# Performance work log

Hardware: AMD Instinct MI355X
Metric: run time of the kernel (lower is better)

## Reference

```python
import jax, jax.numpy as jnp
import numpy as np

D_MODEL, D_HIDDEN, N_EXPERTS, TOP_K = 1024, 2048, 8, 2
B, T = 4, 2048


def setup_inputs() -> dict:
    key = jax.random.key(0)
    ks = jax.random.split(key, 9)
    s_d = 1.0 / np.sqrt(D_MODEL)
    s_h = 1.0 / np.sqrt(D_HIDDEN)
    return {
        "x": jax.random.normal(ks[0], (B, T, D_MODEL), jnp.float32),
        "gate_w": jax.random.normal(ks[1], (D_MODEL, N_EXPERTS), jnp.float32) * s_d,
        "gate_b": jnp.zeros((N_EXPERTS,), jnp.float32),
        "w1": jax.random.normal(ks[2], (N_EXPERTS, D_MODEL, D_HIDDEN), jnp.float32) * s_d,
        "b1": jnp.zeros((N_EXPERTS, D_HIDDEN), jnp.float32),
        "w2": jax.random.normal(ks[3], (N_EXPERTS, D_MODEL, D_HIDDEN), jnp.float32) * s_d,
        "b2": jnp.zeros((N_EXPERTS, D_HIDDEN), jnp.float32),
        "w3": jax.random.normal(ks[4], (N_EXPERTS, D_HIDDEN, D_MODEL), jnp.float32) * s_h,
        "b3": jnp.zeros((N_EXPERTS, D_MODEL), jnp.float32),
    }


def _moe_forward(x, gate_w, gate_b, w1, b1, w2, b2, w3, b3):
    # Router: [B, T, E]
    router_logits = x @ gate_w + gate_b
    top_k_logits, top_k_indices = jax.lax.top_k(router_logits, TOP_K)  # [B,T,K]
    top_k_probs = jax.nn.softmax(top_k_logits, axis=-1)

    # Dense all-expert SwiGLU (matches original, which runs every expert on full batch)
    h = jax.nn.silu(jnp.einsum('btd,edh->bteh', x, w1) + b1) * (
        jnp.einsum('btd,edh->bteh', x, w2) + b2)
    expert_out = jnp.einsum('bteh,ehd->bted', h, w3) + b3  # [B,T,E,D]

    # Combine: gather routed experts' outputs and weight by top-k probs
    gathered = jnp.take_along_axis(expert_out, top_k_indices[:, :, :, None], axis=2)  # [B,T,K,D]
    output = jnp.sum(top_k_probs[:, :, :, None] * gathered, axis=2)

    # Load-balance auxiliary loss
    gate_probs = jax.nn.softmax(router_logits, axis=-1).reshape(-1, N_EXPERTS)
    importance = gate_probs.mean(axis=0)
    idx_flat = top_k_indices.reshape(-1)
    load = jnp.bincount(idx_flat, length=N_EXPERTS).astype(jnp.float32) / idx_flat.size
    aux_loss = jnp.sum(importance * load) * N_EXPERTS
    return output, aux_loss


def reference(x, gate_w, gate_b, w1, b1, w2, b2, w3, b3):
    return _moe_forward(x, gate_w, gate_b, w1, b1, w2, b2, w3, b3)
```

## Files before the change

kernel.cpp:

```cpp
#include <hip/hip_runtime.h>
#include <stdint.h>


#define NTOK     8192
#define DM       1024
#define DH       2048
#define NEXP     8
#define NPAIR    16384
#define TILE_M   128
#define GRID_M   136
#define WC_ROWS  (GRID_M * TILE_M)

typedef _Float16 half8 __attribute__((ext_vector_type(8)));
typedef float    f32x4 __attribute__((ext_vector_type(4)));
typedef unsigned int u32;

__device__ __forceinline__ void gload16(const void* g, void* l) {
  __builtin_amdgcn_global_load_lds(
      (const __attribute__((address_space(1))) u32*)g,
      (__attribute__((address_space(3))) u32*)l, 16, 0, 0);
}

__global__ void init_kernel(float4* __restrict__ out4, int n4, float* __restrict__ aux,
                            int* __restrict__ rtok, float* __restrict__ rprob,
                            int* __restrict__ ctrl) {
  int gid = blockIdx.x * 256 + threadIdx.x;
  int stride = gridDim.x * 256;
  float4 z4 = {0.f, 0.f, 0.f, 0.f};
  for (int i = gid; i < n4; i += stride) out4[i] = z4;
  for (int i = gid; i < WC_ROWS; i += stride) { rtok[i] = -1; rprob[i] = 0.f; }
  if (gid < 64) ctrl[gid] = 0;
  if (gid == 0) *aux = 0.f;
}

template <bool SPLIT>
__global__ __launch_bounds__(256) void transpose_cvt_kernel(
    const float* __restrict__ w1, const float* __restrict__ w2, const float* __restrict__ w3,
    _Float16* __restrict__ w1h, _Float16* __restrict__ w1l,
    _Float16* __restrict__ w2h, _Float16* __restrict__ w2l,
    _Float16* __restrict__ w3h, _Float16* __restrict__ w3l) {
  int z = blockIdx.z;
  int R = (z == 2) ? DH : DM;
  int C = (z == 2) ? DM : DH;
  const float* in = (z == 0) ? w1 : (z == 1) ? w2 : w3;
  _Float16* outh  = (z == 0) ? w1h : (z == 1) ? w2h : w3h;
  _Float16* outl  = (z == 0) ? w1l : (z == 1) ? w2l : w3l;
  size_t ebase = (size_t)blockIdx.y * R * C;
  in += ebase;
  int tilesC = C >> 5;
  int tr = blockIdx.x / tilesC, tc = blockIdx.x % tilesC;
  int r0 = tr << 7, c0 = tc << 5;
  __shared__ float tsh[32][129];
  int tx = threadIdx.x, ty = threadIdx.y;
#pragma unroll
  for (int i = 0; i < 16; i++) {
    int r = ty + i * 8;
    tsh[tx][r] = in[(size_t)(r0 + r) * C + c0 + tx];
  }
  __syncthreads();
  int tid = ty * 32 + tx;
  int c = tid >> 3, g = tid & 7;
  const float* trow = &tsh[c][g * 16];
  _Float16 thi[16], tlo[16];
#pragma unroll
  for (int j = 0; j < 16; j++) {
    float v = trow[j];
    _Float16 hi = (_Float16)v;
    thi[j] = hi;
    if (SPLIT) tlo[j] = (_Float16)(v - (float)hi);
  }
  size_t dsto = ebase + (size_t)(c0 + c) * R + r0 + g * 16;
  half8* dh = (half8*)(outh + dsto);
  dh[0] = *(half8*)&thi[0];
  dh[1] = *(half8*)&thi[8];
  if (SPLIT) {
    half8* dl = (half8*)(outl + dsto);
    dl[0] = *(half8*)&tlo[0];
    dl[1] = *(half8*)&tlo[8];
  }
}

template <bool SPLIT>
__global__ __launch_bounds__(256) void router_kernel(
    const float* __restrict__ x, const float* __restrict__ gw, const float* __restrict__ gb,
    float* __restrict__ g_imp, int* __restrict__ g_cnt,
    int* __restrict__ tok_e, float* __restrict__ tok_p,
    _Float16* __restrict__ xhi, _Float16* __restrict__ xlo) {
  __shared__ float s_imp[8];
  __shared__ int   s_cnt[8];
  int t = threadIdx.x;
  if (t < 8) { s_imp[t] = 0.f; s_cnt[t] = 0; }
  __syncthreads();
  int wave = t >> 6, lane = t & 63;
  int tok = blockIdx.x * 4 + wave;
  const float4* xr = (const float4*)(x + (size_t)tok * DM);
  float acc[8] = {0.f,0.f,0.f,0.f,0.f,0.f,0.f,0.f};
  _Float16 hh[16], ll[16];
#pragma unroll
  for (int j = 0; j < 4; j++) {
    float4 v = xr[lane * 4 + j];
    const float* gw0 = gw + (size_t)(lane * 16 + j * 4) * 8;
#pragma unroll
    for (int e = 0; e < 8; e++)
      acc[e] += v.x * gw0[e] + v.y * gw0[8 + e] + v.z * gw0[16 + e] + v.w * gw0[24 + e];
    float vv[4] = {v.x, v.y, v.z, v.w};
#pragma unroll
    for (int q = 0; q < 4; q++) {
      _Float16 hi = (_Float16)vv[q];
      hh[j * 4 + q] = hi;
      if (SPLIT) ll[j * 4 + q] = (_Float16)(vv[q] - (float)hi);
    }
  }
  size_t xoff = (size_t)tok * DM + lane * 16;
  half8* xo = (half8*)(xhi + xoff);
  xo[0] = *(half8*)&hh[0];
  xo[1] = *(half8*)&hh[8];
  if (SPLIT) {
    half8* xl = (half8*)(xlo + xoff);
    xl[0] = *(half8*)&ll[0];
    xl[1] = *(half8*)&ll[8];
  }
#pragma unroll
  for (int off = 32; off > 0; off >>= 1) {
#pragma unroll
    for (int e = 0; e < 8; e++) acc[e] += __shfl_xor(acc[e], off, 64);
  }
  if (lane == 0) {
    float l[8];
#pragma unroll
    for (int e = 0; e < 8; e++) l[e] = acc[e] + gb[e];
    float v0 = l[0]; int i0 = 0;
#pragma unroll
    for (int e = 1; e < 8; e++) if (l[e] > v0) { v0 = l[e]; i0 = e; }
    float v1 = -3.4e38f; int i1 = -1;
#pragma unroll
    for (int e = 0; e < 8; e++) {
      if (e != i0 && l[e] > v1) { v1 = l[e]; i1 = e; }
    }
    float s = 0.f, p[8];
#pragma unroll
    for (int e = 0; e < 8; e++) { p[e] = expf(l[e] - v0); s += p[e]; }
    float inv = 1.f / s;
#pragma unroll
    for (int e = 0; e < 8; e++) atomicAdd(&s_imp[e], p[e] * inv);
    float e1 = expf(v1 - v0);
    float p0 = 1.f / (1.f + e1);
    tok_e[tok * 2] = i0;  tok_e[tok * 2 + 1] = i1;
    tok_p[tok * 2] = p0;  tok_p[tok * 2 + 1] = e1 * p0;
    atomicAdd(&s_cnt[i0], 1); atomicAdd(&s_cnt[i1], 1);
  }
  __syncthreads();
  if (t < 8) { atomicAdd(&g_imp[t], s_imp[t]); atomicAdd(&g_cnt[t], s_cnt[t]); }
}

__global__ void offsets_aux_kernel(const float* __restrict__ g_imp, const int* __restrict__ g_cnt,
                                   int* __restrict__ segoff, float* __restrict__ aux_out) {
  if (threadIdx.x == 0 && blockIdx.x == 0) {
    int off = 0;
    segoff[0] = 0;
    double aux = 0.0;
    for (int e = 0; e < 8; e++) {
      off += ((g_cnt[e] + TILE_M - 1) >> 7) << 7;
      segoff[e + 1] = off;
      aux += (double)g_imp[e] * (double)g_cnt[e];
    }
    aux_out[0] = (float)(aux * 8.0 / ((double)NTOK * (double)NPAIR));
  }
}

__global__ __launch_bounds__(256) void scatter_rows_kernel(
    const int* __restrict__ tok_e, const float* __restrict__ tok_p,
    const int* __restrict__ segoff, int* __restrict__ cursor,
    int* __restrict__ rtok, float* __restrict__ rprob, int* __restrict__ inv) {
  __shared__ int lcnt[8], lbase[8];
  int t = threadIdx.x;
  if (t < 8) lcnt[t] = 0;
  __syncthreads();
  int i = blockIdx.x * 256 + t;
  int e = tok_e[i];
  int lpos = atomicAdd(&lcnt[e], 1);
  __syncthreads();
  if (t < 8) lbase[t] = (lcnt[t] > 0) ? atomicAdd(&cursor[t], lcnt[t]) : 0;
  __syncthreads();
  int r = segoff[e] + lbase[e] + lpos;
  rtok[r]  = i >> 1;
  rprob[r] = tok_p[i];
  inv[i]   = r;
}

template <bool SPLIT>
__global__ __launch_bounds__(256) void gemm1_kernel(
    const _Float16* __restrict__ xhi, const _Float16* __restrict__ xlo,
    const _Float16* __restrict__ w1h, const _Float16* __restrict__ w1l,
    const _Float16* __restrict__ w2h, const _Float16* __restrict__ w2l,
    const float* __restrict__ b1, const float* __restrict__ b2,
    const int* __restrict__ rtok, const int* __restrict__ segoff,
    _Float16* __restrict__ hhi, _Float16* __restrict__ hlo) {
  int dflat = blockIdx.y * 136 + blockIdx.x;
  int xcd = dflat & 7, j = dflat >> 3;
  int wy = xcd * 2 + (j >= 136 ? 1 : 0);
  int wx = (j >= 136) ? j - 136 : j;
  int mbase = wx * TILE_M;
  if (mbase >= segoff[8]) return;
  int e = 0;
  while (mbase >= segoff[e + 1]) e++;
  int nbase = wy * 128;

  extern __shared__ char smem[];
  _Float16* Ah  = (_Float16*)smem;
  _Float16* B1h = Ah  + 4096;
  _Float16* B2h = B1h + 4096;
  _Float16* Al  = B2h + 4096;
  _Float16* B1l = Al  + 4096;
  _Float16* B2l = B1l + 4096;

  int t = threadIdx.x;
  int lane = t & 63, wave = t >> 6;
  int wr = wave >> 1, wc = wave & 1;

  int r0 = t >> 2, part = t & 3;
  int r1 = 64 + r0;
  int tokA0 = rtok[mbase + r0]; if (tokA0 < 0) tokA0 = 0;
  int tokA1 = rtok[mbase + r1]; if (tokA1 < 0) tokA1 = 0;
  size_t offA0 = (size_t)tokA0 * DM + part * 8;
  size_t offA1 = (size_t)tokA1 * DM + part * 8;
  size_t offB0 = ((size_t)e * DH + nbase + r0) * DM + part * 8;
  size_t offB1 = ((size_t)e * DH + nbase + r1) * DM + part * 8;
  int l0 = wave * 1024, l1 = 4096 + wave * 1024;

  f32x4 uacc[4][4], vacc[4][4];
#pragma unroll
  for (int a = 0; a < 4; a++)
#pragma unroll
    for (int b = 0; b < 4; b++) { uacc[a][b] = {0.f,0.f,0.f,0.f}; vacc[a][b] = {0.f,0.f,0.f,0.f}; }

  for (int kk = 0; kk < DM; kk += 32) {
    gload16(xhi + offA0 + kk, (char*)Ah  + l0);
    gload16(xhi + offA1 + kk, (char*)Ah  + l1);
    gload16(w1h + offB0 + kk, (char*)B1h + l0);
    gload16(w1h + offB1 + kk, (char*)B1h + l1);
    gload16(w2h + offB0 + kk, (char*)B2h + l0);
    gload16(w2h + offB1 + kk, (char*)B2h + l1);
    if (SPLIT) {
      gload16(xlo + offA0 + kk, (char*)Al  + l0);
      gload16(xlo + offA1 + kk, (char*)Al  + l1);
      gload16(w1l + offB0 + kk, (char*)B1l + l0);
      gload16(w1l + offB1 + kk, (char*)B1l + l1);
      gload16(w2l + offB0 + kk, (char*)B2l + l0);
      gload16(w2l + offB1 + kk, (char*)B2l + l1);
    }
    __syncthreads();
    int kpos = (lane >> 4) * 8;
    half8 ah[4], al[4];
#pragma unroll
    for (int i = 0; i < 4; i++) {
      int rowA = wr * 64 + i * 16 + (lane & 15);
      ah[i] = *(const half8*)&Ah[rowA * 32 + kpos];
      if (SPLIT) al[i] = *(const half8*)&Al[rowA * 32 + kpos];
    }
    {
      half8 bh[4], bl[4];
#pragma unroll
      for (int i = 0; i < 4; i++) {
        int rowB = wc * 64 + i * 16 + (lane & 15);
        bh[i] = *(const half8*)&B1h[rowB * 32 + kpos];
        if (SPLIT) bl[i] = *(const half8*)&B1l[rowB * 32 + kpos];
      }
#pragma unroll
      for (int mi = 0; mi < 4; mi++)
#pragma unroll
        for (int ni = 0; ni < 4; ni++) {
          uacc[mi][ni] = __builtin_amdgcn_mfma_f32_16x16x32_f16(ah[mi], bh[ni], uacc[mi][ni], 0, 0, 0);
          if (SPLIT) {
            uacc[mi][ni] = __builtin_amdgcn_mfma_f32_16x16x32_f16(ah[mi], bl[ni], uacc[mi][ni], 0, 0, 0);
            uacc[mi][ni] = __builtin_amdgcn_mfma_f32_16x16x32_f16(al[mi], bh[ni], uacc[mi][ni], 0, 0, 0);
          }
        }
    }
    {
      half8 bh[4], bl[4];
#pragma unroll
      for (int i = 0; i < 4; i++) {
        int rowB = wc * 64 + i * 16 + (lane & 15);
        bh[i] = *(const half8*)&B2h[rowB * 32 + kpos];
        if (SPLIT) bl[i] = *(const half8*)&B2l[rowB * 32 + kpos];
      }
#pragma unroll
      for (int mi = 0; mi < 4; mi++)
#pragma unroll
        for (int ni = 0; ni < 4; ni++) {
          vacc[mi][ni] = __builtin_amdgcn_mfma_f32_16x16x32_f16(ah[mi], bh[ni], vacc[mi][ni], 0, 0, 0);
          if (SPLIT) {
            vacc[mi][ni] = __builtin_amdgcn_mfma_f32_16x16x32_f16(ah[mi], bl[ni], vacc[mi][ni], 0, 0, 0);
            vacc[mi][ni] = __builtin_amdgcn_mfma_f32_16x16x32_f16(al[mi], bh[ni], vacc[mi][ni], 0, 0, 0);
          }
        }
    }
    __syncthreads();
  }

  const float* b1e = b1 + (size_t)e * DH;
  const float* b2e = b2 + (size_t)e * DH;
#pragma unroll
  for (int mi = 0; mi < 4; mi++)
#pragma unroll
    for (int ni = 0; ni < 4; ni++)
#pragma unroll
      for (int r = 0; r < 4; r++) {
        int row = mbase + wr * 64 + mi * 16 + (lane >> 4) * 4 + r;
        int col = nbase + wc * 64 + ni * 16 + (lane & 15);
        float u = uacc[mi][ni][r] + b1e[col];
        float v = vacc[mi][ni][r] + b2e[col];
        float hv = u / (1.f + expf(-u)) * v;
        _Float16 hi = (_Float16)hv;
        hhi[(size_t)row * DH + col] = hi;
        if (SPLIT) hlo[(size_t)row * DH + col] = (_Float16)(hv - (float)hi);
      }
}

template <bool SPLIT, bool WRITE_Y>
__global__ __launch_bounds__(256) void gemm2_kernel(
    const _Float16* __restrict__ hhi, const _Float16* __restrict__ hlo,
    const _Float16* __restrict__ w3h, const _Float16* __restrict__ w3l,
    const float* __restrict__ b3, const int* __restrict__ rtok,
    const float* __restrict__ rprob, const int* __restrict__ segoff,
    float* __restrict__ ybuf, float* __restrict__ out) {
  int dflat = blockIdx.y * 136 + blockIdx.x;
  int xcd = dflat & 7, j = dflat >> 3;
  int mbase = j * TILE_M;
  if (mbase >= segoff[8]) return;
  int e = 0;
  while (mbase >= segoff[e + 1]) e++;
  int nbase = xcd * 128;

  extern __shared__ char smem[];
  _Float16* Ah = (_Float16*)smem;
  _Float16* Bh = Ah + 4096;
  _Float16* Al = Bh + 4096;
  _Float16* Bl = Al + 4096;

  int t = threadIdx.x;
  int lane = t & 63, wave = t >> 6;
  int wr = wave >> 1, wc = wave & 1;

  int r0 = t >> 2, part = t & 3;
  int r1 = 64 + r0;
  size_t offA0 = (size_t)(mbase + r0) * DH + part * 8;
  size_t offA1 = (size_t)(mbase + r1) * DH + part * 8;
  size_t offB0 = ((size_t)e * DM + nbase + r0) * DH + part * 8;
  size_t offB1 = ((size_t)e * DM + nbase + r1) * DH + part * 8;
  int l0 = wave * 1024, l1 = 4096 + wave * 1024;

  f32x4 acc[4][4];
#pragma unroll
  for (int a = 0; a < 4; a++)
#pragma unroll
    for (int b = 0; b < 4; b++) acc[a][b] = {0.f,0.f,0.f,0.f};

  for (int kk = 0; kk < DH; kk += 32) {
    gload16(hhi + offA0 + kk, (char*)Ah + l0);
    gload16(hhi + offA1 + kk, (char*)Ah + l1);
    gload16(w3h + offB0 + kk, (char*)Bh + l0);
    gload16(w3h + offB1 + kk, (char*)Bh + l1);
    if (SPLIT) {
      gload16(hlo + offA0 + kk, (char*)Al + l0);
      gload16(hlo + offA1 + kk, (char*)Al + l1);
      gload16(w3l + offB0 + kk, (char*)Bl + l0);
      gload16(w3l + offB1 + kk, (char*)Bl + l1);
    }
    __syncthreads();
    int kpos = (lane >> 4) * 8;
    half8 ah[4], al[4], bh[4], bl[4];
#pragma unroll
    for (int i = 0; i < 4; i++) {
      int rowA = wr * 64 + i * 16 + (lane & 15);
      int rowB = wc * 64 + i * 16 + (lane & 15);
      ah[i] = *(const half8*)&Ah[rowA * 32 + kpos];
      bh[i] = *(const half8*)&Bh[rowB * 32 + kpos];
      if (SPLIT) {
        al[i] = *(const half8*)&Al[rowA * 32 + kpos];
        bl[i] = *(const half8*)&Bl[rowB * 32 + kpos];
      }
    }
#pragma unroll
    for (int mi = 0; mi < 4; mi++)
#pragma unroll
      for (int ni = 0; ni < 4; ni++) {
        acc[mi][ni] = __builtin_amdgcn_mfma_f32_16x16x32_f16(ah[mi], bh[ni], acc[mi][ni], 0, 0, 0);
        if (SPLIT) {
          acc[mi][ni] = __builtin_amdgcn_mfma_f32_16x16x32_f16(ah[mi], bl[ni], acc[mi][ni], 0, 0, 0);
          acc[mi][ni] = __builtin_amdgcn_mfma_f32_16x16x32_f16(al[mi], bh[ni], acc[mi][ni], 0, 0, 0);
        }
      }
    __syncthreads();
  }

  const float* b3e = b3 + (size_t)e * DM;
#pragma unroll
  for (int mi = 0; mi < 4; mi++)
#pragma unroll
    for (int r = 0; r < 4; r++) {
      int row = mbase + wr * 64 + mi * 16 + (lane >> 4) * 4 + r;
      if (WRITE_Y) {
#pragma unroll
        for (int ni = 0; ni < 4; ni++) {
          int col = nbase + wc * 64 + ni * 16 + (lane & 15);
          ybuf[(size_t)row * DM + col] = acc[mi][ni][r] + b3e[col];
        }
      } else {
        int tok = rtok[row];
        if (tok < 0) continue;
        float pr = rprob[row];
#pragma unroll
        for (int ni = 0; ni < 4; ni++) {
          int col = nbase + wc * 64 + ni * 16 + (lane & 15);
          float val = (acc[mi][ni][r] + b3e[col]) * pr;
          atomicAdd(&out[(size_t)tok * DM + col], val);
        }
      }
    }
}

__global__ __launch_bounds__(256) void combine_kernel(
    const float4* __restrict__ ybuf, const int* __restrict__ inv,
    const float* __restrict__ tok_p, float4* __restrict__ out) {
  int gid = blockIdx.x * 256 + threadIdx.x;
  int tok = gid >> 8;
  int c4  = gid & 255;
  int r0 = inv[tok * 2], r1 = inv[tok * 2 + 1];
  float p0 = tok_p[tok * 2], p1 = tok_p[tok * 2 + 1];
  float4 a = ybuf[(size_t)r0 * 256 + c4];
  float4 b = ybuf[(size_t)r1 * 256 + c4];
  float4 o;
  o.x = p0 * a.x + p1 * b.x;
  o.y = p0 * a.y + p1 * b.y;
  o.z = p0 * a.z + p1 * b.z;
  o.w = p0 * a.w + p1 * b.w;
  out[gid] = o;
}

extern "C" void kernel_launch(void* const* d_in, const int* in_sizes, int n_in,
                              void* d_out, int out_size, void* d_ws, size_t ws_size,
                              hipStream_t stream) {
  const float* x      = (const float*)d_in[0];
  const float* gate_w = (const float*)d_in[1];
  const float* gate_b = (const float*)d_in[2];
  const float* w1     = (const float*)d_in[3];
  const float* b1     = (const float*)d_in[4];
  const float* w2     = (const float*)d_in[5];
  const float* b2     = (const float*)d_in[6];
  const float* w3     = (const float*)d_in[7];
  const float* b3     = (const float*)d_in[8];
  float* out = (float*)d_out;

  const size_t SZ_XH = (size_t)NTOK * DM * 2;
  const size_t SZ_W  = (size_t)NEXP * DM * DH * 2;
  const size_t SZ_H  = (size_t)WC_ROWS * DH * 2;
  const size_t SZ_Y  = (size_t)WC_ROWS * DM * 4;
  const size_t SZ_RT = (size_t)WC_ROWS * 4;
  const size_t SZ_NP = (size_t)NPAIR * 4;

  char* ws = (char*)d_ws;
  float* g_imp  = (float*)(ws + 0);
  int*   g_cnt  = (int*)(ws + 32);
  int*   cursor = (int*)(ws + 64);
  int*   segoff = (int*)(ws + 96);

  size_t o = 256;
  _Float16 *A_xhi, *A_xlo, *A_w1h, *A_w1l, *A_w2h, *A_w2l, *A_w3h, *A_w3l, *A_hhi, *A_hlo;
  int *A_rtok, *A_toke, *A_inv; float *A_rprob, *A_tokp, *A_y;
  A_xhi = (_Float16*)(ws + o); o += SZ_XH;
  A_xlo = (_Float16*)(ws + o); o += SZ_XH;
  A_w1h = (_Float16*)(ws + o); o += SZ_W;
  A_w1l = (_Float16*)(ws + o); o += SZ_W;
  A_w2h = (_Float16*)(ws + o); o += SZ_W;
  A_w2l = (_Float16*)(ws + o); o += SZ_W;
  A_w3h = (_Float16*)(ws + o); o += SZ_W;
  A_w3l = (_Float16*)(ws + o); o += SZ_W;
  A_hhi = (_Float16*)(ws + o); o += SZ_H;
  A_hlo = (_Float16*)(ws + o); o += SZ_H;
  A_rtok = (int*)(ws + o);   o += SZ_RT;
  A_rprob= (float*)(ws + o); o += SZ_RT;
  A_toke = (int*)(ws + o);   o += SZ_NP;
  A_tokp = (float*)(ws + o); o += SZ_NP;
  A_inv  = (int*)(ws + o);   o += SZ_NP;
  A_y    = (float*)(ws + o); o += SZ_Y;
  size_t offA = o;

  o = 256;
  _Float16 *B_xh, *B_w1, *B_w2, *B_w3, *B_h;
  int *B_rtok, *B_toke, *B_inv; float *B_rprob, *B_tokp, *B_y;
  B_xh = (_Float16*)(ws + o); o += SZ_XH;
  B_w1 = (_Float16*)(ws + o); o += SZ_W;
  B_w2 = (_Float16*)(ws + o); o += SZ_W;
  B_w3 = (_Float16*)(ws + o); o += SZ_W;
  B_h  = (_Float16*)(ws + o); o += SZ_H;
  B_rtok = (int*)(ws + o);   o += SZ_RT;
  B_rprob= (float*)(ws + o); o += SZ_RT;
  B_toke = (int*)(ws + o);   o += SZ_NP;
  B_tokp = (float*)(ws + o); o += SZ_NP;
  B_inv  = (int*)(ws + o);   o += SZ_NP;
  size_t offC = o;
  B_y    = (float*)(ws + o); o += SZ_Y;
  size_t offB = o;

  int mode = (ws_size >= offA) ? 2 : (ws_size >= offB) ? 1 : 0;
  (void)offC;

  if (mode == 2) {
    init_kernel<<<2048, 256, 0, stream>>>((float4*)out, NTOK * DM / 4,
                                          out + (size_t)NTOK * DM, A_rtok, A_rprob, (int*)ws);
    transpose_cvt_kernel<true><<<dim3(512, 8, 3), dim3(32, 8), 0, stream>>>(
        w1, w2, w3, A_w1h, A_w1l, A_w2h, A_w2l, A_w3h, A_w3l);
    router_kernel<true><<<NTOK / 4, 256, 0, stream>>>(x, gate_w, gate_b, g_imp, g_cnt,
                                                      A_toke, A_tokp, A_xhi, A_xlo);
    offsets_aux_kernel<<<1, 64, 0, stream>>>(g_imp, g_cnt, segoff, out + (size_t)NTOK * DM);
    scatter_rows_kernel<<<NPAIR / 256, 256, 0, stream>>>(A_toke, A_tokp, segoff, cursor,
                                                         A_rtok, A_rprob, A_inv);
    gemm1_kernel<true><<<dim3(136, 16), 256, 49152, stream>>>(
        A_xhi, A_xlo, A_w1h, A_w1l, A_w2h, A_w2l, b1, b2, A_rtok, segoff, A_hhi, A_hlo);
    gemm2_kernel<true, true><<<dim3(136, 8), 256, 32768, stream>>>(
        A_hhi, A_hlo, A_w3h, A_w3l, b3, A_rtok, A_rprob, segoff, A_y, out);
    combine_kernel<<<NTOK * DM / 4 / 256, 256, 0, stream>>>((const float4*)A_y, A_inv,
                                                            A_tokp, (float4*)out);
  } else {
    init_kernel<<<2048, 256, 0, stream>>>((float4*)out, NTOK * DM / 4,
                                          out + (size_t)NTOK * DM, B_rtok, B_rprob, (int*)ws);
    transpose_cvt_kernel<false><<<dim3(512, 8, 3), dim3(32, 8), 0, stream>>>(
        w1, w2, w3, B_w1, nullptr, B_w2, nullptr, B_w3, nullptr);
    router_kernel<false><<<NTOK / 4, 256, 0, stream>>>(x, gate_w, gate_b, g_imp, g_cnt,
                                                       B_toke, B_tokp, B_xh, nullptr);
    offsets_aux_kernel<<<1, 64, 0, stream>>>(g_imp, g_cnt, segoff, out + (size_t)NTOK * DM);
    scatter_rows_kernel<<<NPAIR / 256, 256, 0, stream>>>(B_toke, B_tokp, segoff, cursor,
                                                         B_rtok, B_rprob, B_inv);
    gemm1_kernel<false><<<dim3(136, 16), 256, 24576, stream>>>(
        B_xh, nullptr, B_w1, nullptr, B_w2, nullptr, b1, b2, B_rtok, segoff, B_h, nullptr);
    if (mode == 1) {
      gemm2_kernel<false, true><<<dim3(136, 8), 256, 16384, stream>>>(
          B_h, nullptr, B_w3, nullptr, b3, B_rtok, B_rprob, segoff, B_y, out);
      combine_kernel<<<NTOK * DM / 4 / 256, 256, 0, stream>>>((const float4*)B_y, B_inv,
                                                              B_tokp, (float4*)out);
    } else {
      gemm2_kernel<false, false><<<dim3(136, 8), 256, 16384, stream>>>(
          B_h, nullptr, B_w3, nullptr, b3, B_rtok, B_rprob, segoff, B_y, out);
    }
  }
}
```

Baseline: 822.2 us.

## Drop split-fp16 compensation, double-buffer LDS with swizzle in both GEMMs

Removes the hi/lo fp16 split path, so the GEMMs run one MFMA per tile instead of three and move half the operand bytes. Both GEMMs gain double-buffered LDS staging with prefetch of the next K slice, an XOR swizzle on global-to-LDS placement against bank conflicts, and s_setprio around the MFMA blocks. SiLU now uses __expf. The trade is lower accuracy, since plain fp16 inputs replace the compensated product and may push results past the tolerance.

```diff
diff --git a/kernel.cpp b/kernel.cpp
--- a/kernel.cpp
+++ b/kernel.cpp
@@ -33,18 +33,14 @@
   if (gid == 0) *aux = 0.f;
 }
 
-template <bool SPLIT>
 __global__ __launch_bounds__(256) void transpose_cvt_kernel(
     const float* __restrict__ w1, const float* __restrict__ w2, const float* __restrict__ w3,
-    _Float16* __restrict__ w1h, _Float16* __restrict__ w1l,
-    _Float16* __restrict__ w2h, _Float16* __restrict__ w2l,
-    _Float16* __restrict__ w3h, _Float16* __restrict__ w3l) {
+    _Float16* __restrict__ w1t, _Float16* __restrict__ w2t, _Float16* __restrict__ w3t) {
   int z = blockIdx.z;
   int R = (z == 2) ? DH : DM;
   int C = (z == 2) ? DM : DH;
   const float* in = (z == 0) ? w1 : (z == 1) ? w2 : w3;
-  _Float16* outh  = (z == 0) ? w1h : (z == 1) ? w2h : w3h;
-  _Float16* outl  = (z == 0) ? w1l : (z == 1) ? w2l : w3l;
+  _Float16*   out = (z == 0) ? w1t : (z == 1) ? w2t : w3t;
   size_t ebase = (size_t)blockIdx.y * R * C;
   in += ebase;
   int tilesC = C >> 5;
@@ -61,31 +57,18 @@
   int tid = ty * 32 + tx;
   int c = tid >> 3, g = tid & 7;
   const float* trow = &tsh[c][g * 16];
-  _Float16 thi[16], tlo[16];
-#pragma unroll
-  for (int j = 0; j < 16; j++) {
-    float v = trow[j];
-    _Float16 hi = (_Float16)v;
-    thi[j] = hi;
-    if (SPLIT) tlo[j] = (_Float16)(v - (float)hi);
-  }
-  size_t dsto = ebase + (size_t)(c0 + c) * R + r0 + g * 16;
-  half8* dh = (half8*)(outh + dsto);
-  dh[0] = *(half8*)&thi[0];
-  dh[1] = *(half8*)&thi[8];
-  if (SPLIT) {
-    half8* dl = (half8*)(outl + dsto);
-    dl[0] = *(half8*)&tlo[0];
-    dl[1] = *(half8*)&tlo[8];
-  }
-}
-
-template <bool SPLIT>
+  _Float16 tmp[16];
+#pragma unroll
+  for (int j = 0; j < 16; j++) tmp[j] = (_Float16)trow[j];
+  half8* dst = (half8*)(out + ebase + (size_t)(c0 + c) * R + r0 + g * 16);
+  dst[0] = *(half8*)&tmp[0];
+  dst[1] = *(half8*)&tmp[8];
+}
+
 __global__ __launch_bounds__(256) void router_kernel(
     const float* __restrict__ x, const float* __restrict__ gw, const float* __restrict__ gb,
     float* __restrict__ g_imp, int* __restrict__ g_cnt,
-    int* __restrict__ tok_e, float* __restrict__ tok_p,
-    _Float16* __restrict__ xhi, _Float16* __restrict__ xlo) {
+    int* __restrict__ tok_e, float* __restrict__ tok_p, _Float16* __restrict__ xh) {
   __shared__ float s_imp[8];
   __shared__ int   s_cnt[8];
   int t = threadIdx.x;
@@ -95,7 +78,7 @@
   int tok = blockIdx.x * 4 + wave;
   const float4* xr = (const float4*)(x + (size_t)tok * DM);
   float acc[8] = {0.f,0.f,0.f,0.f,0.f,0.f,0.f,0.f};
-  _Float16 hh[16], ll[16];
+  _Float16 hh[16];
 #pragma unroll
   for (int j = 0; j < 4; j++) {
     float4 v = xr[lane * 4 + j];
@@ -103,23 +86,12 @@
 #pragma unroll
     for (int e = 0; e < 8; e++)
       acc[e] += v.x * gw0[e] + v.y * gw0[8 + e] + v.z * gw0[16 + e] + v.w * gw0[24 + e];
-    float vv[4] = {v.x, v.y, v.z, v.w};
-#pragma unroll
-    for (int q = 0; q < 4; q++) {
-      _Float16 hi = (_Float16)vv[q];
-      hh[j * 4 + q] = hi;
-      if (SPLIT) ll[j * 4 + q] = (_Float16)(vv[q] - (float)hi);
-    }
-  }
-  size_t xoff = (size_t)tok * DM + lane * 16;
-  half8* xo = (half8*)(xhi + xoff);
+    hh[j * 4 + 0] = (_Float16)v.x; hh[j * 4 + 1] = (_Float16)v.y;
+    hh[j * 4 + 2] = (_Float16)v.z; hh[j * 4 + 3] = (_Float16)v.w;
+  }
+  half8* xo = (half8*)(xh + (size_t)tok * DM + lane * 16);
   xo[0] = *(half8*)&hh[0];
   xo[1] = *(half8*)&hh[8];
-  if (SPLIT) {
-    half8* xl = (half8*)(xlo + xoff);
-    xl[0] = *(half8*)&ll[0];
-    xl[1] = *(half8*)&ll[8];
-  }
 #pragma unroll
   for (int off = 32; off > 0; off >>= 1) {
 #pragma unroll
@@ -188,14 +160,11 @@
   inv[i]   = r;
 }
 
-template <bool SPLIT>
 __global__ __launch_bounds__(256) void gemm1_kernel(
-    const _Float16* __restrict__ xhi, const _Float16* __restrict__ xlo,
-    const _Float16* __restrict__ w1h, const _Float16* __restrict__ w1l,
-    const _Float16* __restrict__ w2h, const _Float16* __restrict__ w2l,
-    const float* __restrict__ b1, const float* __restrict__ b2,
-    const int* __restrict__ rtok, const int* __restrict__ segoff,
-    _Float16* __restrict__ hhi, _Float16* __restrict__ hlo) {
+    const _Float16* __restrict__ xh, const _Float16* __restrict__ w1t,
+    const _Float16* __restrict__ w2t, const float* __restrict__ b1,
+    const float* __restrict__ b2, const int* __restrict__ rtok,
+    const int* __restrict__ segoff, _Float16* __restrict__ hbuf) {
   int dflat = blockIdx.y * 136 + blockIdx.x;
   int xcd = dflat & 7, j = dflat >> 3;
   int wy = xcd * 2 + (j >= 136 ? 1 : 0);
@@ -206,26 +175,21 @@
   while (mbase >= segoff[e + 1]) e++;
   int nbase = wy * 128;
 
-  extern __shared__ char smem[];
-  _Float16* Ah  = (_Float16*)smem;
-  _Float16* B1h = Ah  + 4096;
-  _Float16* B2h = B1h + 4096;
-  _Float16* Al  = B2h + 4096;
-  _Float16* B1l = Al  + 4096;
-  _Float16* B2l = B1l + 4096;
+  __shared__ _Float16 smem[2][3][4096];
 
   int t = threadIdx.x;
   int lane = t & 63, wave = t >> 6;
   int wr = wave >> 1, wc = wave & 1;
 
-  int r0 = t >> 2, part = t & 3;
+  int r0 = t >> 2;
   int r1 = 64 + r0;
+  int partg = (t & 3) ^ ((t >> 3) & 3);
   int tokA0 = rtok[mbase + r0]; if (tokA0 < 0) tokA0 = 0;
   int tokA1 = rtok[mbase + r1]; if (tokA1 < 0) tokA1 = 0;
-  size_t offA0 = (size_t)tokA0 * DM + part * 8;
-  size_t offA1 = (size_t)tokA1 * DM + part * 8;
-  size_t offB0 = ((size_t)e * DH + nbase + r0) * DM + part * 8;
-  size_t offB1 = ((size_t)e * DH + nbase + r1) * DM + part * 8;
+  size_t offA0 = (size_t)tokA0 * DM + partg * 8;
+  size_t offA1 = (size_t)tokA1 * DM + partg * 8;
+  size_t offB0 = ((size_t)e * DH + nbase + r0) * DM + partg * 8;
+  size_t offB1 = ((size_t)e * DH + nbase + r1) * DM + partg * 8;
   int l0 = wave * 1024, l1 = 4096 + wave * 1024;
 
   f32x4 uacc[4][4], vacc[4][4];
@@ -234,69 +198,63 @@
 #pragma unroll
     for (int b = 0; b < 4; b++) { uacc[a][b] = {0.f,0.f,0.f,0.f}; vacc[a][b] = {0.f,0.f,0.f,0.f}; }
 
+  auto STAGE = [&](int buf, int kk) {
+    char* base = (char*)&smem[buf][0][0];
+    gload16(xh  + offA0 + kk, base + l0);
+    gload16(xh  + offA1 + kk, base + l1);
+    gload16(w1t + offB0 + kk, base + 8192 + l0);
+    gload16(w1t + offB1 + kk, base + 8192 + l1);
+    gload16(w2t + offB0 + kk, base + 16384 + l0);
+    gload16(w2t + offB1 + kk, base + 16384 + l1);
+  };
+
+  int kgrp = lane >> 4;
+  int sOff = ((kgrp ^ ((lane >> 1) & 3)) << 3);
+
+  STAGE(0, 0);
+  __syncthreads();
+  int cur = 0;
   for (int kk = 0; kk < DM; kk += 32) {
-    gload16(xhi + offA0 + kk, (char*)Ah  + l0);
-    gload16(xhi + offA1 + kk, (char*)Ah  + l1);
-    gload16(w1h + offB0 + kk, (char*)B1h + l0);
-    gload16(w1h + offB1 + kk, (char*)B1h + l1);
-    gload16(w2h + offB0 + kk, (char*)B2h + l0);
-    gload16(w2h + offB1 + kk, (char*)B2h + l1);
-    if (SPLIT) {
-      gload16(xlo + offA0 + kk, (char*)Al  + l0);
-      gload16(xlo + offA1 + kk, (char*)Al  + l1);
-      gload16(w1l + offB0 + kk, (char*)B1l + l0);
-      gload16(w1l + offB1 + kk, (char*)B1l + l1);
-      gload16(w2l + offB0 + kk, (char*)B2l + l0);
-      gload16(w2l + offB1 + kk, (char*)B2l + l1);
-    }
-    __syncthreads();
-    int kpos = (lane >> 4) * 8;
-    half8 ah[4], al[4];
+    if (kk + 32 < DM) STAGE(cur ^ 1, kk + 32);
+    const _Float16* Ac  = &smem[cur][0][0];
+    const _Float16* B1c = &smem[cur][1][0];
+    const _Float16* B2c = &smem[cur][2][0];
+    half8 af[4];
 #pragma unroll
     for (int i = 0; i < 4; i++) {
       int rowA = wr * 64 + i * 16 + (lane & 15);
-      ah[i] = *(const half8*)&Ah[rowA * 32 + kpos];
-      if (SPLIT) al[i] = *(const half8*)&Al[rowA * 32 + kpos];
-    }
+      af[i] = *(const half8*)&Ac[rowA * 32 + sOff];
+    }
+    __builtin_amdgcn_s_setprio(1);
     {
-      half8 bh[4], bl[4];
+      half8 bf[4];
 #pragma unroll
       for (int i = 0; i < 4; i++) {
         int rowB = wc * 64 + i * 16 + (lane & 15);
-        bh[i] = *(const half8*)&B1h[rowB * 32 + kpos];
-        if (SPLIT) bl[i] = *(const half8*)&B1l[rowB * 32 + kpos];
+        bf[i] = *(const half8*)&B1c[rowB * 32 + sOff];
       }
 #pragma unroll
       for (int mi = 0; mi < 4; mi++)
 #pragma unroll
-        for (int ni = 0; ni < 4; ni++) {
-          uacc[mi][ni] = __builtin_amdgcn_mfma_f32_16x16x32_f16(ah[mi], bh[ni], uacc[mi][ni], 0, 0, 0);
-          if (SPLIT) {
-            uacc[mi][ni] = __builtin_amdgcn_mfma_f32_16x16x32_f16(ah[mi], bl[ni], uacc[mi][ni], 0, 0, 0);
-            uacc[mi][ni] = __builtin_amdgcn_mfma_f32_16x16x32_f16(al[mi], bh[ni], uacc[mi][ni], 0, 0, 0);
-          }
-        }
+        for (int ni = 0; ni < 4; ni++)
+          uacc[mi][ni] = __builtin_amdgcn_mfma_f32_16x16x32_f16(af[mi], bf[ni], uacc[mi][ni], 0, 0, 0);
     }
     {
-      half8 bh[4], bl[4];
+      half8 bf[4];
 #pragma unroll
       for (int i = 0; i < 4; i++) {
         int rowB = wc * 64 + i * 16 + (lane & 15);
-        bh[i] = *(const half8*)&B2h[rowB * 32 + kpos];
-        if (SPLIT) bl[i] = *(const half8*)&B2l[rowB * 32 + kpos];
+        bf[i] = *(const half8*)&B2c[rowB * 32 + sOff];
       }
 #pragma unroll
       for (int mi = 0; mi < 4; mi++)
 #pragma unroll
-        for (int ni = 0; ni < 4; ni++) {
-          vacc[mi][ni] = __builtin_amdgcn_mfma_f32_16x16x32_f16(ah[mi], bh[ni], vacc[mi][ni], 0, 0, 0);
-          if (SPLIT) {
-            vacc[mi][ni] = __builtin_amdgcn_mfma_f32_16x16x32_f16(ah[mi], bl[ni], vacc[mi][ni], 0, 0, 0);
-            vacc[mi][ni] = __builtin_amdgcn_mfma_f32_16x16x32_f16(al[mi], bh[ni], vacc[mi][ni], 0, 0, 0);
-          }
-        }
-    }
+        for (int ni = 0; ni < 4; ni++)
+          vacc[mi][ni] = __builtin_amdgcn_mfma_f32_16x16x32_f16(af[mi], bf[ni], vacc[mi][ni], 0, 0, 0);
+    }
+    __builtin_amdgcn_s_setprio(0);
     __syncthreads();
+    cur ^= 1;
   }
 
   const float* b1e = b1 + (size_t)e * DH;
@@ -311,17 +269,14 @@
         int col = nbase + wc * 64 + ni * 16 + (lane & 15);
         float u = uacc[mi][ni][r] + b1e[col];
         float v = vacc[mi][ni][r] + b2e[col];
-        float hv = u / (1.f + expf(-u)) * v;
-        _Float16 hi = (_Float16)hv;
-        hhi[(size_t)row * DH + col] = hi;
-        if (SPLIT) hlo[(size_t)row * DH + col] = (_Float16)(hv - (float)hi);
+        float hv = u / (1.f + __expf(-u)) * v;
+        hbuf[(size_t)row * DH + col] = (_Float16)hv;
       }
 }
 
-template <bool SPLIT, bool WRITE_Y>
+template <bool WRITE_Y>
 __global__ __launch_bounds__(256) void gemm2_kernel(
-    const _Float16* __restrict__ hhi, const _Float16* __restrict__ hlo,
-    const _Float16* __restrict__ w3h, const _Float16* __restrict__ w3l,
+    const _Float16* __restrict__ hbuf, const _Float16* __restrict__ w3t,
     const float* __restrict__ b3, const int* __restrict__ rtok,
     const float* __restrict__ rprob, const int* __restrict__ segoff,
     float* __restrict__ ybuf, float* __restrict__ out) {
@@ -333,22 +288,19 @@
   while (mbase >= segoff[e + 1]) e++;
   int nbase = xcd * 128;
 
-  extern __shared__ char smem[];
-  _Float16* Ah = (_Float16*)smem;
-  _Float16* Bh = Ah + 4096;
-  _Float16* Al = Bh + 4096;
-  _Float16* Bl = Al + 4096;
+  __shared__ _Float16 smem[2][2][4096];
 
   int t = threadIdx.x;
   int lane = t & 63, wave = t >> 6;
   int wr = wave >> 1, wc = wave & 1;
 
-  int r0 = t >> 2, part = t & 3;
+  int r0 = t >> 2;
   int r1 = 64 + r0;
-  size_t offA0 = (size_t)(mbase + r0) * DH + part * 8;
-  size_t offA1 = (size_t)(mbase + r1) * DH + part * 8;
-  size_t offB0 = ((size_t)e * DM + nbase + r0) * DH + part * 8;
-  size_t offB1 = ((size_t)e * DM + nbase + r1) * DH + part * 8;
+  int partg = (t & 3) ^ ((t >> 3) & 3);
+  size_t offA0 = (size_t)(mbase + r0) * DH + partg * 8;
+  size_t offA1 = (size_t)(mbase + r1) * DH + partg * 8;
+  size_t offB0 = ((size_t)e * DM + nbase + r0) * DH + partg * 8;
+  size_t offB1 = ((size_t)e * DM + nbase + r1) * DH + partg * 8;
   int l0 = wave * 1024, l1 = 4096 + wave * 1024;
 
   f32x4 acc[4][4];
@@ -357,42 +309,41 @@
 #pragma unroll
     for (int b = 0; b < 4; b++) acc[a][b] = {0.f,0.f,0.f,0.f};
 
+  auto STAGE = [&](int buf, int kk) {
+    char* base = (char*)&smem[buf][0][0];
+    gload16(hbuf + offA0 + kk, base + l0);
+    gload16(hbuf + offA1 + kk, base + l1);
+    gload16(w3t + offB0 + kk, base + 8192 + l0);
+    gload16(w3t + offB1 + kk, base + 8192 + l1);
+  };
+
+  int kgrp = lane >> 4;
+  int sOff = ((kgrp ^ ((lane >> 1) & 3)) << 3);
+
+  STAGE(0, 0);
+  __syncthreads();
+  int cur = 0;
   for (int kk = 0; kk < DH; kk += 32) {
-    gload16(hhi + offA0 + kk, (char*)Ah + l0);
-    gload16(hhi + offA1 + kk, (char*)Ah + l1);
-    gload16(w3h + offB0 + kk, (char*)Bh + l0);
-    gload16(w3h + offB1 + kk, (char*)Bh + l1);
-    if (SPLIT) {
-      gload16(hlo + offA0 + kk, (char*)Al + l0);
-      gload16(hlo + offA1 + kk, (char*)Al + l1);
-      gload16(w3l + offB0 + kk, (char*)Bl + l0);
-      gload16(w3l + offB1 + kk, (char*)Bl + l1);
-    }
-    __syncthreads();
-    int kpos = (lane >> 4) * 8;
-    half8 ah[4], al[4], bh[4], bl[4];
+    if (kk + 32 < DH) STAGE(cur ^ 1, kk + 32);
+    const _Float16* Ac = &smem[cur][0][0];
+    const _Float16* Bc = &smem[cur][1][0];
+    half8 af[4], bf[4];
 #pragma unroll
     for (int i = 0; i < 4; i++) {
       int rowA = wr * 64 + i * 16 + (lane & 15);
       int rowB = wc * 64 + i * 16 + (lane & 15);
-      ah[i] = *(const half8*)&Ah[rowA * 32 + kpos];
-      bh[i] = *(const half8*)&Bh[rowB * 32 + kpos];
-      if (SPLIT) {
-        al[i] = *(const half8*)&Al[rowA * 32 + kpos];
-        bl[i] = *(const half8*)&Bl[rowB * 32 + kpos];
-      }
-    }
+      af[i] = *(const half8*)&Ac[rowA * 32 + sOff];
+      bf[i] = *(const half8*)&Bc[rowB * 32 + sOff];
+    }
+    __builtin_amdgcn_s_setprio(1);
 #pragma unroll
     for (int mi = 0; mi < 4; mi++)
 #pragma unroll
-      for (int ni = 0; ni < 4; ni++) {
-        acc[mi][ni] = __builtin_amdgcn_mfma_f32_16x16x32_f16(ah[mi], bh[ni], acc[mi][ni], 0, 0, 0);
-        if (SPLIT) {
-          acc[mi][ni] = __builtin_amdgcn_mfma_f32_16x16x32_f16(ah[mi], bl[ni], acc[mi][ni], 0, 0, 0);
-          acc[mi][ni] = __builtin_amdgcn_mfma_f32_16x16x32_f16(al[mi], bh[ni], acc[mi][ni], 0, 0, 0);
-        }
-      }
+      for (int ni = 0; ni < 4; ni++)
+        acc[mi][ni] = __builtin_amdgcn_mfma_f32_16x16x32_f16(af[mi], bf[ni], acc[mi][ni], 0, 0, 0);
+    __builtin_amdgcn_s_setprio(0);
     __syncthreads();
+    cur ^= 1;
   }
 
   const float* b3e = b3 + (size_t)e * DM;
@@ -467,82 +418,37 @@
   int*   segoff = (int*)(ws + 96);
 
   size_t o = 256;
-  _Float16 *A_xhi, *A_xlo, *A_w1h, *A_w1l, *A_w2h, *A_w2l, *A_w3h, *A_w3l, *A_hhi, *A_hlo;
-  int *A_rtok, *A_toke, *A_inv; float *A_rprob, *A_tokp, *A_y;
-  A_xhi = (_Float16*)(ws + o); o += SZ_XH;
-  A_xlo = (_Float16*)(ws + o); o += SZ_XH;
-  A_w1h = (_Float16*)(ws + o); o += SZ_W;
-  A_w1l = (_Float16*)(ws + o); o += SZ_W;
-  A_w2h = (_Float16*)(ws + o); o += SZ_W;
-  A_w2l = (_Float16*)(ws + o); o += SZ_W;
-  A_w3h = (_Float16*)(ws + o); o += SZ_W;
-  A_w3l = (_Float16*)(ws + o); o += SZ_W;
-  A_hhi = (_Float16*)(ws + o); o += SZ_H;
-  A_hlo = (_Float16*)(ws + o); o += SZ_H;
-  A_rtok = (int*)(ws + o);   o += SZ_RT;
-  A_rprob= (float*)(ws + o); o += SZ_RT;
-  A_toke = (int*)(ws + o);   o += SZ_NP;
-  A_tokp = (float*)(ws + o); o += SZ_NP;
-  A_inv  = (int*)(ws + o);   o += SZ_NP;
-  A_y    = (float*)(ws + o); o += SZ_Y;
-  size_t offA = o;
-
-  o = 256;
-  _Float16 *B_xh, *B_w1, *B_w2, *B_w3, *B_h;
-  int *B_rtok, *B_toke, *B_inv; float *B_rprob, *B_tokp, *B_y;
-  B_xh = (_Float16*)(ws + o); o += SZ_XH;
-  B_w1 = (_Float16*)(ws + o); o += SZ_W;
-  B_w2 = (_Float16*)(ws + o); o += SZ_W;
-  B_w3 = (_Float16*)(ws + o); o += SZ_W;
-  B_h  = (_Float16*)(ws + o); o += SZ_H;
-  B_rtok = (int*)(ws + o);   o += SZ_RT;
-  B_rprob= (float*)(ws + o); o += SZ_RT;
-  B_toke = (int*)(ws + o);   o += SZ_NP;
-  B_tokp = (float*)(ws + o); o += SZ_NP;
-  B_inv  = (int*)(ws + o);   o += SZ_NP;
+  _Float16* xh  = (_Float16*)(ws + o); o += SZ_XH;
+  _Float16* w1t = (_Float16*)(ws + o); o += SZ_W;
+  _Float16* w2t = (_Float16*)(ws + o); o += SZ_W;
+  _Float16* w3t = (_Float16*)(ws + o); o += SZ_W;
+  _Float16* hb  = (_Float16*)(ws + o); o += SZ_H;
+  int*   rtok  = (int*)(ws + o);   o += SZ_RT;
+  float* rprob = (float*)(ws + o); o += SZ_RT;
+  int*   tok_e = (int*)(ws + o);   o += SZ_NP;
+  float* tok_p = (float*)(ws + o); o += SZ_NP;
+  int*   inv   = (int*)(ws + o);   o += SZ_NP;
   size_t offC = o;
-  B_y    = (float*)(ws + o); o += SZ_Y;
+  float* ybuf  = (float*)(ws + o); o += SZ_Y;
   size_t offB = o;
-
-  int mode = (ws_size >= offA) ? 2 : (ws_size >= offB) ? 1 : 0;
+  bool use_y = (ws_size >= offB);
   (void)offC;
 
-  if (mode == 2) {
-    init_kernel<<<2048, 256, 0, stream>>>((float4*)out, NTOK * DM / 4,
-                                          out + (size_t)NTOK * DM, A_rtok, A_rprob, (int*)ws);
-    transpose_cvt_kernel<true><<<dim3(512, 8, 3), dim3(32, 8), 0, stream>>>(
-        w1, w2, w3, A_w1h, A_w1l, A_w2h, A_w2l, A_w3h, A_w3l);
-    router_kernel<true><<<NTOK / 4, 256, 0, stream>>>(x, gate_w, gate_b, g_imp, g_cnt,
-                                                      A_toke, A_tokp, A_xhi, A_xlo);
-    offsets_aux_kernel<<<1, 64, 0, stream>>>(g_imp, g_cnt, segoff, out + (size_t)NTOK * DM);
-    scatter_rows_kernel<<<NPAIR / 256, 256, 0, stream>>>(A_toke, A_tokp, segoff, cursor,
-                                                         A_rtok, A_rprob, A_inv);
-    gemm1_kernel<true><<<dim3(136, 16), 256, 49152, stream>>>(
-        A_xhi, A_xlo, A_w1h, A_w1l, A_w2h, A_w2l, b1, b2, A_rtok, segoff, A_hhi, A_hlo);
-    gemm2_kernel<true, true><<<dim3(136, 8), 256, 32768, stream>>>(
-        A_hhi, A_hlo, A_w3h, A_w3l, b3, A_rtok, A_rprob, segoff, A_y, out);
-    combine_kernel<<<NTOK * DM / 4 / 256, 256, 0, stream>>>((const float4*)A_y, A_inv,
-                                                            A_tokp, (float4*)out);
+  init_kernel<<<2048, 256, 0, stream>>>((float4*)out, NTOK * DM / 4,
+                                        out + (size_t)NTOK * DM, rtok, rprob, (int*)ws);
+  transpose_cvt_kernel<<<dim3(512, 8, 3), dim3(32, 8), 0, stream>>>(w1, w2, w3, w1t, w2t, w3t);
+  router_kernel<<<NTOK / 4, 256, 0, stream>>>(x, gate_w, gate_b, g_imp, g_cnt, tok_e, tok_p, xh);
+  offsets_aux_kernel<<<1, 64, 0, stream>>>(g_imp, g_cnt, segoff, out + (size_t)NTOK * DM);
+  scatter_rows_kernel<<<NPAIR / 256, 256, 0, stream>>>(tok_e, tok_p, segoff, cursor,
+                                                       rtok, rprob, inv);
+  gemm1_kernel<<<dim3(136, 16), 256, 0, stream>>>(xh, w1t, w2t, b1, b2, rtok, segoff, hb);
+  if (use_y) {
+    gemm2_kernel<true><<<dim3(136, 8), 256, 0, stream>>>(hb, w3t, b3, rtok, rprob, segoff,
+                                                         ybuf, out);
+    combine_kernel<<<NTOK * DM / 4 / 256, 256, 0, stream>>>((const float4*)ybuf, inv, tok_p,
+                                                            (float4*)out);
   } else {
-    init_kernel<<<2048, 256, 0, stream>>>((float4*)out, NTOK * DM / 4,
-                                          out + (size_t)NTOK * DM, B_rtok, B_rprob, (int*)ws);
-    transpose_cvt_kernel<false><<<dim3(512, 8, 3), dim3(32, 8), 0, stream>>>(
-        w1, w2, w3, B_w1, nullptr, B_w2, nullptr, B_w3, nullptr);
-    router_kernel<false><<<NTOK / 4, 256, 0, stream>>>(x, gate_w, gate_b, g_imp, g_cnt,
-                                                       B_toke, B_tokp, B_xh, nullptr);
-    offsets_aux_kernel<<<1, 64, 0, stream>>>(g_imp, g_cnt, segoff, out + (size_t)NTOK * DM);
-    scatter_rows_kernel<<<NPAIR / 256, 256, 0, stream>>>(B_toke, B_tokp, segoff, cursor,
-                                                         B_rtok, B_rprob, B_inv);
-    gemm1_kernel<false><<<dim3(136, 16), 256, 24576, stream>>>(
-        B_xh, nullptr, B_w1, nullptr, B_w2, nullptr, b1, b2, B_rtok, segoff, B_h, nullptr);
-    if (mode == 1) {
-      gemm2_kernel<false, true><<<dim3(136, 8), 256, 16384, stream>>>(
-          B_h, nullptr, B_w3, nullptr, b3, B_rtok, B_rprob, segoff, B_y, out);
-      combine_kernel<<<NTOK * DM / 4 / 256, 256, 0, stream>>>((const float4*)B_y, B_inv,
-                                                              B_tokp, (float4*)out);
-    } else {
-      gemm2_kernel<false, false><<<dim3(136, 8), 256, 16384, stream>>>(
-          B_h, nullptr, B_w3, nullptr, b3, B_rtok, B_rprob, segoff, B_y, out);
-    }
-  }
-}
+    gemm2_kernel<false><<<dim3(136, 8), 256, 0, stream>>>(hb, w3t, b3, rtok, rprob, segoff,
+                                                          ybuf, out);
+  }
+}
```

Measured after the change: 699.2 us. 1.18x faster.
